# Kernel tuning notes

Hardware: AMD Instinct MI355X
Metric: run time of the kernel (lower is better)

## Reference

```python
import jax, jax.numpy as jnp
import numpy as np

N, E, DIN, DH, H, L = 8192, 32768, 1024, 256, 8, 3
NEG_SLOPE = 0.2  # PyG GATv2Conv default


def setup_inputs() -> dict:
    key = jax.random.key(0)
    ks = jax.random.split(key, 16)
    s = 0.05
    p = {}
    p["x"] = jax.random.normal(ks[0], (N, DIN), jnp.float32)
    p["edge_index"] = jax.random.randint(ks[1], (2, E), 0, N, jnp.int32)
    p["edge_attr"] = jax.random.randint(ks[2], (E,), 0, 5, jnp.int32)
    p["node_types"] = jax.random.randint(ks[3], (N,), 0, 5, jnp.int32)
    # input_proj (input_dim != hidden_dim so it is a Linear)
    p["W_in"] = jax.random.normal(ks[4], (DIN, DH), jnp.float32) * s
    p["b_in"] = jnp.zeros((DH,), jnp.float32)
    p["node_emb"] = jax.random.normal(ks[5], (5, DH), jnp.float32) * s
    p["edge_emb"] = jax.random.normal(ks[6], (5, DH), jnp.float32) * s
    # per-layer GATv2 params, stacked over L layers
    p["Wl"] = jax.random.normal(ks[7], (L, DH, H * DH), jnp.float32) * s   # lin_l
    p["bl"] = jnp.zeros((L, H * DH), jnp.float32)
    p["Wr"] = jax.random.normal(ks[8], (L, DH, H * DH), jnp.float32) * s   # lin_r
    p["br"] = jnp.zeros((L, H * DH), jnp.float32)
    p["We"] = jax.random.normal(ks[9], (L, DH, H * DH), jnp.float32) * s   # lin_edge (no bias)
    p["att"] = jax.random.normal(ks[10], (L, H, DH), jnp.float32) * s
    p["b_gat"] = jnp.zeros((L, DH), jnp.float32)                            # out bias (concat=False)
    p["W_out"] = jax.random.normal(ks[11], (DH, DH), jnp.float32) * s
    p["b_out"] = jnp.zeros((DH,), jnp.float32)
    return p


def _gatv2(h, src, dst, ea, Wl, bl, Wr, br, We, att, bias):
    n = h.shape[0]
    # add self loops; edge_attr fill_value='mean' = segment-mean of incoming edge attrs
    loop = jnp.arange(n, dtype=src.dtype)
    cnt = jax.ops.segment_sum(jnp.ones(dst.shape, jnp.float32), dst, num_segments=n)
    loop_ea = jax.ops.segment_sum(ea, dst, num_segments=n) / jnp.maximum(cnt, 1.0)[:, None]
    src2 = jnp.concatenate([src, loop])
    dst2 = jnp.concatenate([dst, loop])
    ea2 = jnp.concatenate([ea, loop_ea], axis=0)
    xl = (h @ Wl + bl).reshape(n, H, DH)   # source transform
    xr = (h @ Wr + br).reshape(n, H, DH)   # target transform
    ee = (ea2 @ We).reshape(-1, H, DH)     # edge transform [E2,H,C]
    z = jax.nn.leaky_relu(xl[src2] + xr[dst2] + ee, NEG_SLOPE)   # [E2,H,C]
    logits = jnp.einsum('ehc,hc->eh', z, att)                    # [E2,H]
    # numerically stable segment softmax over edges sharing a target node
    lmax = jax.ops.segment_max(logits, dst2, num_segments=n)     # [N,H]
    pnum = jnp.exp(logits - lmax[dst2])
    alpha = pnum / jax.ops.segment_sum(pnum, dst2, num_segments=n)[dst2]
    out = jax.ops.segment_sum(alpha[:, :, None] * xl[src2], dst2, num_segments=n)  # [N,H,C]
    return out.mean(axis=1) + bias          # concat=False -> head mean + bias


def reference(x, edge_index, edge_attr, node_types, W_in, b_in, node_emb, edge_emb,
              Wl, bl, Wr, br, We, att, b_gat, W_out, b_out):
    src, dst = edge_index[0], edge_index[1]
    h = x @ W_in + b_in + node_emb[node_types]
    for l in range(L):
        ea = edge_emb[edge_attr]
        h = jax.nn.relu(_gatv2(h, src, dst, ea, Wl[l], bl[l], Wr[l], br[l], We[l], att[l], b_gat[l]))
        # dropout p=0.1 is a no-op in eval mode
    return h @ W_out + b_out
```

## Files before the change

### kernel.cpp

```cpp
#include <hip/hip_runtime.h>

#define N_NODES 8192
#define N_EDGES 32768
#define D_IN    1024
#define DH      256
#define NH      8
#define HD      2048
#define NL      3
#define NT      5
#define NEG     0.2f

typedef __bf16 bf16x8 __attribute__((ext_vector_type(8)));
typedef float  f32x4  __attribute__((ext_vector_type(4)));
typedef unsigned short ushort8 __attribute__((ext_vector_type(8)));

static __device__ __forceinline__ unsigned short f2bf(float f) {
    unsigned u = __float_as_uint(f);
    unsigned r = (u + 0x7FFFu + ((u >> 16) & 1u)) >> 16;
    return (unsigned short)r;
}
static __device__ __forceinline__ float bf2f(unsigned short h) {
    return __uint_as_float(((unsigned)h) << 16);
}
static __device__ __forceinline__ void gload_lds16(const void* g, void* l) {
    __builtin_amdgcn_global_load_lds(
        (const __attribute__((address_space(1))) unsigned*)g,
        (__attribute__((address_space(3))) unsigned*)l, 16, 0, 0);
}

__global__ __launch_bounds__(256) void split_act8(
    const float* __restrict__ X, unsigned short* __restrict__ A3,
    int MK8, int k8shift)
{
    int idx = blockIdx.x * 256 + threadIdx.x;
    if (idx >= MK8) return;
    int K8 = 1 << k8shift;
    int K = K8 << 3;
    int m = idx >> k8shift, k8 = idx & (K8 - 1);
    const float* xp = X + (size_t)m * K + k8 * 8;
    float4 v0 = *(const float4*)xp;
    float4 v1 = *(const float4*)(xp + 4);
    float vv[8] = {v0.x, v0.y, v0.z, v0.w, v1.x, v1.y, v1.z, v1.w};
    ushort8 hi, lo;
#pragma unroll
    for (int j = 0; j < 8; j++) {
        unsigned short h = f2bf(vv[j]);
        hi[j] = h;
        lo[j] = f2bf(vv[j] - bf2f(h));
    }
    size_t b = (size_t)m * 3 * K + k8 * 8;
    *(ushort8*)(A3 + b)         = hi;
    *(ushort8*)(A3 + b + K)     = hi;
    *(ushort8*)(A3 + b + 2 * K) = lo;
}

__global__ __launch_bounds__(256) void split_w(
    const float* __restrict__ W, unsigned short* __restrict__ B3T,
    int K, int N)
{
    __shared__ float t[32][33];
    int k0 = blockIdx.y * 32, n0 = blockIdx.x * 32;
    int tid = threadIdx.x;
    int r = tid >> 5, c = tid & 31;
    for (int rr = r; rr < 32; rr += 8)
        t[rr][c] = W[(size_t)(k0 + rr) * N + n0 + c];
    __syncthreads();
    for (int rr = r; rr < 32; rr += 8) {
        int n = n0 + rr, k = k0 + c;
        float v = t[c][rr];
        unsigned short hu = f2bf(v);
        unsigned short lu = f2bf(v - bf2f(hu));
        size_t b = (size_t)n * 3 * K + k;
        B3T[b]         = hu;
        B3T[b + K]     = lu;
        B3T[b + 2 * K] = hu;
    }
}

__global__ __launch_bounds__(256) void init_c(
    float* __restrict__ C, const float* __restrict__ bias, int MN, int nshift,
    const float* __restrict__ emb, const int* __restrict__ types)
{
    for (int idx = blockIdx.x * 256 + threadIdx.x; idx < MN; idx += gridDim.x * 256) {
        int col = idx & ((1 << nshift) - 1);
        float v = bias[col];
        if (emb) v += emb[types[idx >> nshift] * DH + col];
        C[idx] = v;
    }
}

__global__ __launch_bounds__(256) void gemm_mfma(
    const unsigned short* __restrict__ A3, const unsigned short* __restrict__ B3T,
    const float* __restrict__ bias, float* __restrict__ C,
    int M, int N, int K3, int kslice)
{
    __shared__ unsigned short aLds[128 * 64];
    __shared__ unsigned short bLds[128 * 64];
    const int tid = threadIdx.x;
    const int m0 = blockIdx.y * 128, n0 = blockIdx.x * 128;
    const int lane = tid & 63, w = tid >> 6;
    const int wm = w >> 1, wn = w & 1;
    const int srow8 = lane >> 3;
    const int schunk = lane & 7;
    const int frow = lane & 15, fchunk = lane >> 4;
    const int kt0 = blockIdx.z * kslice;
    const int kt1 = kt0 + kslice;

    f32x4 acc[4][4] = {};

    for (int kt = kt0; kt < kt1; kt += 64) {
#pragma unroll
        for (int q = 0; q < 4; q++) {
            int row = (q * 4 + w) * 8 + srow8;
            int scol = (schunk << 4) ^ ((row & 7) << 4);
            char* ldst_a = (char*)aLds + (q * 4 + w) * 1024;
            char* ldst_b = (char*)bLds + (q * 4 + w) * 1024;
            gload_lds16(A3 + (size_t)(m0 + row) * K3 + kt + (scol >> 1), ldst_a);
            gload_lds16(B3T + (size_t)(n0 + row) * K3 + kt + (scol >> 1), ldst_b);
        }
        __syncthreads();
#pragma unroll
        for (int kh = 0; kh < 2; kh++) {
            const int c = kh * 4 + fchunk;
            bf16x8 af[4], bfr[4];
#pragma unroll
            for (int f = 0; f < 4; f++) {
                int ra = wm * 64 + f * 16 + frow;
                af[f] = *(const bf16x8*)((const char*)aLds + ra * 128 + ((c ^ (ra & 7)) << 4));
                int rb = wn * 64 + f * 16 + frow;
                bfr[f] = *(const bf16x8*)((const char*)bLds + rb * 128 + ((c ^ (rb & 7)) << 4));
            }
#pragma unroll
            for (int i = 0; i < 4; i++)
#pragma unroll
                for (int j = 0; j < 4; j++)
                    acc[i][j] = __builtin_amdgcn_mfma_f32_16x16x32_bf16(
                        af[i], bfr[j], acc[i][j], 0, 0, 0);
        }
        __syncthreads();
    }

    const int ccol = lane & 15, crq = (lane >> 4) * 4;
    if (gridDim.z == 1) {
#pragma unroll
        for (int j = 0; j < 4; j++) {
            int gcol = n0 + wn * 64 + j * 16 + ccol;
            float bv = bias[gcol];
#pragma unroll
            for (int i = 0; i < 4; i++)
#pragma unroll
                for (int r = 0; r < 4; r++) {
                    int grow = m0 + wm * 64 + i * 16 + crq + r;
                    C[(size_t)grow * N + gcol] = acc[i][j][r] + bv;
                }
        }
    } else {
#pragma unroll
        for (int j = 0; j < 4; j++) {
            int gcol = n0 + wn * 64 + j * 16 + ccol;
#pragma unroll
            for (int i = 0; i < 4; i++)
#pragma unroll
                for (int r = 0; r < 4; r++) {
                    int grow = m0 + wm * 64 + i * 16 + crq + r;
                    atomicAdd(&C[(size_t)grow * N + gcol], acc[i][j][r]);
                }
        }
    }
}

__global__ __launch_bounds__(256) void e5_kernel(
    const float* __restrict__ eemb, const float* __restrict__ We,
    float* __restrict__ E5)
{
    int col = blockIdx.x * 256 + threadIdx.x;
    int t = blockIdx.y;
    float acc = 0.f;
    for (int k = 0; k < DH; k++) acc += eemb[t * DH + k] * We[(size_t)k * HD + col];
    E5[(size_t)t * HD + col] = acc;
}

__global__ void deg_hist(const int* __restrict__ dst, const int* __restrict__ attr,
                         int* cnt, int* hist)
{
    int e = blockIdx.x * 256 + threadIdx.x;
    if (e < N_EDGES) {
        int d = dst[e];
        atomicAdd(&cnt[d], 1);
        atomicAdd(&hist[d * NT + attr[e]], 1);
    }
}

__global__ __launch_bounds__(256) void scan_kernel(const int* __restrict__ cnt,
                                                   int* __restrict__ rowptr)
{
    __shared__ int part[256];
    int tid = threadIdx.x;
    int base = tid * 32, s = 0;
    for (int i = 0; i < 32; i++) s += cnt[base + i];
    part[tid] = s;
    __syncthreads();
    for (int off = 1; off < 256; off <<= 1) {
        int v = (tid >= off) ? part[tid - off] : 0;
        __syncthreads();
        part[tid] += v;
        __syncthreads();
    }
    int run = (tid == 0) ? 0 : part[tid - 1];
    for (int i = 0; i < 32; i++) { rowptr[base + i] = run; run += cnt[base + i]; }
    if (tid == 255) rowptr[N_NODES] = run;
}

__global__ void csr_fill(const int* __restrict__ dst, const int* __restrict__ rowptr,
                         int* fillc, int* __restrict__ csr)
{
    int e = blockIdx.x * 256 + threadIdx.x;
    if (e < N_EDGES) {
        int d = dst[e];
        int p = atomicAdd(&fillc[d], 1);
        csr[rowptr[d] + p] = e;
    }
}

__global__ __launch_bounds__(256) void gat_online(
    const float* __restrict__ xl, const float* __restrict__ xr,
    const float* __restrict__ E5, const float* __restrict__ att,
    const int* __restrict__ csr, const int* __restrict__ rowptr,
    const int* __restrict__ cnt, const int* __restrict__ src,
    const int* __restrict__ attr, const int* __restrict__ hist,
    const float* __restrict__ bgat, float* __restrict__ hout)
{
    const int n = blockIdx.x, tid = threadIdx.x;
    const int h = tid >> 5, cb = tid & 31;
    const int base = h * DH + cb * 8;
    __shared__ float outs[NH][DH];

    const int deg = cnt[n];
    const int r0 = rowptr[n];

    float4 xr0 = *(const float4*)(xr + (size_t)n * HD + base);
    float4 xr1 = *(const float4*)(xr + (size_t)n * HD + base + 4);
    float4 at0 = *(const float4*)(att + base);
    float4 at1 = *(const float4*)(att + base + 4);

    float m = -1e30f, d = 0.f;
    float O0 = 0.f, O1 = 0.f, O2 = 0.f, O3 = 0.f;
    float O4 = 0.f, O5 = 0.f, O6 = 0.f, O7 = 0.f;

    for (int i = 0; i <= deg; i++) {
        const bool isloop = (i == deg);
        int s, a = 0;
        if (isloop) { s = n; }
        else { int e = csr[r0 + i]; s = src[e]; a = attr[e]; }

        const float* xp = xl + (size_t)s * HD + base;
        float4 v0 = *(const float4*)xp;
        float4 v1 = *(const float4*)(xp + 4);

        float4 e0, e1;
        if (isloop) {
            float inv = 1.f / fmaxf((float)deg, 1.f);
            e0 = make_float4(0.f, 0.f, 0.f, 0.f);
            e1 = make_float4(0.f, 0.f, 0.f, 0.f);
#pragma unroll
            for (int t = 0; t < NT; t++) {
                float wt = inv * (float)hist[n * NT + t];
                float4 q0 = *(const float4*)(E5 + (size_t)t * HD + base);
                float4 q1 = *(const float4*)(E5 + (size_t)t * HD + base + 4);
                e0.x += wt * q0.x; e0.y += wt * q0.y; e0.z += wt * q0.z; e0.w += wt * q0.w;
                e1.x += wt * q1.x; e1.y += wt * q1.y; e1.z += wt * q1.z; e1.w += wt * q1.w;
            }
        } else {
            e0 = *(const float4*)(E5 + (size_t)a * HD + base);
            e1 = *(const float4*)(E5 + (size_t)a * HD + base + 4);
        }

        float z, lsum = 0.f;
        z = v0.x + xr0.x + e0.x; z = (z >= 0.f) ? z : NEG * z; lsum += z * at0.x;
        z = v0.y + xr0.y + e0.y; z = (z >= 0.f) ? z : NEG * z; lsum += z * at0.y;
        z = v0.z + xr0.z + e0.z; z = (z >= 0.f) ? z : NEG * z; lsum += z * at0.z;
        z = v0.w + xr0.w + e0.w; z = (z >= 0.f) ? z : NEG * z; lsum += z * at0.w;
        z = v1.x + xr1.x + e1.x; z = (z >= 0.f) ? z : NEG * z; lsum += z * at1.x;
        z = v1.y + xr1.y + e1.y; z = (z >= 0.f) ? z : NEG * z; lsum += z * at1.y;
        z = v1.z + xr1.z + e1.z; z = (z >= 0.f) ? z : NEG * z; lsum += z * at1.z;
        z = v1.w + xr1.w + e1.w; z = (z >= 0.f) ? z : NEG * z; lsum += z * at1.w;

#pragma unroll
        for (int off = 16; off; off >>= 1) lsum += __shfl_xor(lsum, off, 32);

        float nm = fmaxf(m, lsum);
        float scale = __expf(m - nm);
        float p = __expf(lsum - nm);
        O0 = O0 * scale + p * v0.x; O1 = O1 * scale + p * v0.y;
        O2 = O2 * scale + p * v0.z; O3 = O3 * scale + p * v0.w;
        O4 = O4 * scale + p * v1.x; O5 = O5 * scale + p * v1.y;
        O6 = O6 * scale + p * v1.z; O7 = O7 * scale + p * v1.w;
        d = d * scale + p;
        m = nm;
    }

    float invd = 1.f / d;
    float4 w0 = make_float4(O0 * invd, O1 * invd, O2 * invd, O3 * invd);
    float4 w1 = make_float4(O4 * invd, O5 * invd, O6 * invd, O7 * invd);
    *(float4*)(&outs[h][cb * 8])     = w0;
    *(float4*)(&outs[h][cb * 8 + 4]) = w1;
    __syncthreads();

    float o = 0.f;
#pragma unroll
    for (int hh = 0; hh < NH; hh++) o += outs[hh][tid];
    o = o * 0.125f + bgat[tid];
    hout[(size_t)n * DH + tid] = fmaxf(o, 0.f);
}

extern "C" void kernel_launch(void* const* d_in, const int* in_sizes, int n_in,
                              void* d_out, int out_size, void* d_ws, size_t ws_size,
                              hipStream_t stream)
{
    const float* x     = (const float*)d_in[0];
    const int*   eidx  = (const int*)d_in[1];
    const int*   src   = eidx;
    const int*   dst   = eidx + N_EDGES;
    const int*   attr  = (const int*)d_in[2];
    const int*   types = (const int*)d_in[3];
    const float* W_in  = (const float*)d_in[4];
    const float* b_in  = (const float*)d_in[5];
    const float* nemb  = (const float*)d_in[6];
    const float* eemb  = (const float*)d_in[7];
    const float* Wl    = (const float*)d_in[8];
    const float* bl    = (const float*)d_in[9];
    const float* Wr    = (const float*)d_in[10];
    const float* br    = (const float*)d_in[11];
    const float* We    = (const float*)d_in[12];
    const float* att   = (const float*)d_in[13];
    const float* bgat  = (const float*)d_in[14];
    const float* W_out = (const float*)d_in[15];
    const float* b_out = (const float*)d_in[16];
    float* out = (float*)d_out;

    char* ws = (char*)d_ws;
    size_t off = 0;
    auto alloc = [&](size_t bytes) -> void* {
        void* p = ws + off;
        off += (bytes + 255) & ~(size_t)255;
        return p;
    };
    float* h      = (float*)alloc((size_t)N_NODES * DH * 4);
    float* xl     = (float*)alloc((size_t)N_NODES * HD * 4);
    float* xr     = (float*)alloc((size_t)N_NODES * HD * 4);
    float* E5     = (float*)alloc((size_t)NT * HD * 4);
    int* cnt      = (int*)alloc((size_t)N_NODES * 4);
    int* hist     = (int*)alloc((size_t)N_NODES * NT * 4);
    int* rowptr   = (int*)alloc((size_t)(N_NODES + 1) * 4);
    int* fillc    = (int*)alloc((size_t)N_NODES * 4);
    int* csr      = (int*)alloc((size_t)N_EDGES * 4);
    unsigned short* A3  = (unsigned short*)alloc((size_t)N_NODES * 3 * D_IN * 2);
    unsigned short* B3T = (unsigned short*)alloc((size_t)HD * 3 * D_IN * 2);

    hipMemsetAsync(cnt, 0, (size_t)N_NODES * 4, stream);
    hipMemsetAsync(hist, 0, (size_t)N_NODES * NT * 4, stream);
    hipMemsetAsync(fillc, 0, (size_t)N_NODES * 4, stream);

    deg_hist<<<(N_EDGES + 255) / 256, 256, 0, stream>>>(dst, attr, cnt, hist);
    scan_kernel<<<1, 256, 0, stream>>>(cnt, rowptr);
    csr_fill<<<(N_EDGES + 255) / 256, 256, 0, stream>>>(dst, rowptr, fillc, csr);

    split_act8<<<(N_NODES * D_IN / 8 + 255) / 256, 256, 0, stream>>>(
        x, A3, N_NODES * D_IN / 8, 7);
    split_w<<<dim3(DH / 32, D_IN / 32), 256, 0, stream>>>(W_in, B3T, D_IN, DH);
    init_c<<<2048, 256, 0, stream>>>(h, b_in, N_NODES * DH, 8, nemb, types);
    gemm_mfma<<<dim3(DH / 128, N_NODES / 128, 8), 256, 0, stream>>>(
        A3, B3T, nullptr, h, N_NODES, DH, 3 * D_IN, 3 * D_IN / 8);

    for (int l = 0; l < NL; l++) {
        const float* Wl_l = Wl + (size_t)l * DH * HD;
        const float* Wr_l = Wr + (size_t)l * DH * HD;
        const float* We_l = We + (size_t)l * DH * HD;

        split_act8<<<(N_NODES * DH / 8 + 255) / 256, 256, 0, stream>>>(
            h, A3, N_NODES * DH / 8, 5);
        split_w<<<dim3(HD / 32, DH / 32), 256, 0, stream>>>(Wl_l, B3T, DH, HD);
        gemm_mfma<<<dim3(HD / 128, N_NODES / 128, 1), 256, 0, stream>>>(
            A3, B3T, bl + (size_t)l * HD, xl, N_NODES, HD, 3 * DH, 3 * DH);
        split_w<<<dim3(HD / 32, DH / 32), 256, 0, stream>>>(Wr_l, B3T, DH, HD);
        gemm_mfma<<<dim3(HD / 128, N_NODES / 128, 1), 256, 0, stream>>>(
            A3, B3T, br + (size_t)l * HD, xr, N_NODES, HD, 3 * DH, 3 * DH);

        e5_kernel<<<dim3(HD / 256, NT), 256, 0, stream>>>(eemb, We_l, E5);
        gat_online<<<N_NODES, 256, 0, stream>>>(
            xl, xr, E5, att + (size_t)l * NH * DH, csr, rowptr, cnt, src, attr,
            hist, bgat + (size_t)l * DH, h);
    }

    split_act8<<<(N_NODES * DH / 8 + 255) / 256, 256, 0, stream>>>(
        h, A3, N_NODES * DH / 8, 5);
    split_w<<<dim3(DH / 32, DH / 32), 256, 0, stream>>>(W_out, B3T, DH, DH);
    init_c<<<2048, 256, 0, stream>>>(out, b_out, N_NODES * DH, 8, nullptr, nullptr);
    gemm_mfma<<<dim3(DH / 128, N_NODES / 128, 4), 256, 0, stream>>>(
        A3, B3T, nullptr, out, N_NODES, DH, 3 * DH, 3 * DH / 4);
}
```

Baseline: 805.0 us.

## Fuse lin_l and lin_r GEMMs and prefetch next neighbor in GAT aggregation

Concatenates the Wl and Wr projections into a single GEMM producing an interleaved [N, 4096] xl|xr buffer, with per-column bias selection, removing one GEMM launch per layer. The GAT online-softmax loop now loads the next neighbor's xl features before computing the current edge, overlapping gather latency with arithmetic. This costs extra registers and a wider row stride in the gathered buffer.

```diff
diff --git a/kernel.cpp b/kernel.cpp
--- a/kernel.cpp
+++ b/kernel.cpp
@@ -6,6 +6,7 @@
 #define DH      256
 #define NH      8
 #define HD      2048
+#define W2      4096
 #define NL      3
 #define NT      5
 #define NEG     0.2f
@@ -91,8 +92,8 @@
 
 __global__ __launch_bounds__(256) void gemm_mfma(
     const unsigned short* __restrict__ A3, const unsigned short* __restrict__ B3T,
-    const float* __restrict__ bias, float* __restrict__ C,
-    int M, int N, int K3, int kslice)
+    const float* __restrict__ bias, const float* __restrict__ bias2, int nsplit,
+    float* __restrict__ C, int M, int N, int K3, int kslice)
 {
     __shared__ unsigned short aLds[128 * 64];
     __shared__ unsigned short bLds[128 * 64];
@@ -145,7 +146,7 @@
 #pragma unroll
         for (int j = 0; j < 4; j++) {
             int gcol = n0 + wn * 64 + j * 16 + ccol;
-            float bv = bias[gcol];
+            float bv = (gcol < nsplit) ? bias[gcol] : bias2[gcol - nsplit];
 #pragma unroll
             for (int i = 0; i < 4; i++)
 #pragma unroll
@@ -223,12 +224,12 @@
 }
 
 __global__ __launch_bounds__(256) void gat_online(
-    const float* __restrict__ xl, const float* __restrict__ xr,
-    const float* __restrict__ E5, const float* __restrict__ att,
-    const int* __restrict__ csr, const int* __restrict__ rowptr,
-    const int* __restrict__ cnt, const int* __restrict__ src,
-    const int* __restrict__ attr, const int* __restrict__ hist,
-    const float* __restrict__ bgat, float* __restrict__ hout)
+    const float* __restrict__ xlr, const float* __restrict__ E5,
+    const float* __restrict__ att, const int* __restrict__ csr,
+    const int* __restrict__ rowptr, const int* __restrict__ cnt,
+    const int* __restrict__ src, const int* __restrict__ attr,
+    const int* __restrict__ hist, const float* __restrict__ bgat,
+    float* __restrict__ hout)
 {
     const int n = blockIdx.x, tid = threadIdx.x;
     const int h = tid >> 5, cb = tid & 31;
@@ -238,8 +239,8 @@
     const int deg = cnt[n];
     const int r0 = rowptr[n];
 
-    float4 xr0 = *(const float4*)(xr + (size_t)n * HD + base);
-    float4 xr1 = *(const float4*)(xr + (size_t)n * HD + base + 4);
+    float4 xr0 = *(const float4*)(xlr + (size_t)n * W2 + HD + base);
+    float4 xr1 = *(const float4*)(xlr + (size_t)n * W2 + HD + base + 4);
     float4 at0 = *(const float4*)(att + base);
     float4 at1 = *(const float4*)(att + base + 4);
 
@@ -247,43 +248,53 @@
     float O0 = 0.f, O1 = 0.f, O2 = 0.f, O3 = 0.f;
     float O4 = 0.f, O5 = 0.f, O6 = 0.f, O7 = 0.f;
 
+    int a_c;
+    int s_c;
+    if (deg == 0) { s_c = n; a_c = -1; }
+    else { int e0 = csr[r0]; s_c = src[e0]; a_c = attr[e0]; }
+    const float* xp = xlr + (size_t)s_c * W2 + base;
+    float4 v0 = *(const float4*)xp;
+    float4 v1 = *(const float4*)(xp + 4);
+
     for (int i = 0; i <= deg; i++) {
-        const bool isloop = (i == deg);
-        int s, a = 0;
-        if (isloop) { s = n; }
-        else { int e = csr[r0 + i]; s = src[e]; a = attr[e]; }
-
-        const float* xp = xl + (size_t)s * HD + base;
-        float4 v0 = *(const float4*)xp;
-        float4 v1 = *(const float4*)(xp + 4);
-
-        float4 e0, e1;
-        if (isloop) {
+        int a_n = 0;
+        float4 n0 = make_float4(0.f, 0.f, 0.f, 0.f), n1 = n0;
+        if (i < deg) {
+            int s_n;
+            if (i + 1 == deg) { s_n = n; a_n = -1; }
+            else { int e = csr[r0 + i + 1]; s_n = src[e]; a_n = attr[e]; }
+            const float* xq = xlr + (size_t)s_n * W2 + base;
+            n0 = *(const float4*)xq;
+            n1 = *(const float4*)(xq + 4);
+        }
+
+        float4 e0v, e1v;
+        if (a_c < 0) {
             float inv = 1.f / fmaxf((float)deg, 1.f);
-            e0 = make_float4(0.f, 0.f, 0.f, 0.f);
-            e1 = make_float4(0.f, 0.f, 0.f, 0.f);
+            e0v = make_float4(0.f, 0.f, 0.f, 0.f);
+            e1v = make_float4(0.f, 0.f, 0.f, 0.f);
 #pragma unroll
             for (int t = 0; t < NT; t++) {
                 float wt = inv * (float)hist[n * NT + t];
                 float4 q0 = *(const float4*)(E5 + (size_t)t * HD + base);
                 float4 q1 = *(const float4*)(E5 + (size_t)t * HD + base + 4);
-                e0.x += wt * q0.x; e0.y += wt * q0.y; e0.z += wt * q0.z; e0.w += wt * q0.w;
-                e1.x += wt * q1.x; e1.y += wt * q1.y; e1.z += wt * q1.z; e1.w += wt * q1.w;
+                e0v.x += wt * q0.x; e0v.y += wt * q0.y; e0v.z += wt * q0.z; e0v.w += wt * q0.w;
+                e1v.x += wt * q1.x; e1v.y += wt * q1.y; e1v.z += wt * q1.z; e1v.w += wt * q1.w;
             }
         } else {
-            e0 = *(const float4*)(E5 + (size_t)a * HD + base);
-            e1 = *(const float4*)(E5 + (size_t)a * HD + base + 4);
+            e0v = *(const float4*)(E5 + (size_t)a_c * HD + base);
+            e1v = *(const float4*)(E5 + (size_t)a_c * HD + base + 4);
         }
 
         float z, lsum = 0.f;
-        z = v0.x + xr0.x + e0.x; z = (z >= 0.f) ? z : NEG * z; lsum += z * at0.x;
-        z = v0.y + xr0.y + e0.y; z = (z >= 0.f) ? z : NEG * z; lsum += z * at0.y;
-        z = v0.z + xr0.z + e0.z; z = (z >= 0.f) ? z : NEG * z; lsum += z * at0.z;
-        z = v0.w + xr0.w + e0.w; z = (z >= 0.f) ? z : NEG * z; lsum += z * at0.w;
-        z = v1.x + xr1.x + e1.x; z = (z >= 0.f) ? z : NEG * z; lsum += z * at1.x;
-        z = v1.y + xr1.y + e1.y; z = (z >= 0.f) ? z : NEG * z; lsum += z * at1.y;
-        z = v1.z + xr1.z + e1.z; z = (z >= 0.f) ? z : NEG * z; lsum += z * at1.z;
-        z = v1.w + xr1.w + e1.w; z = (z >= 0.f) ? z : NEG * z; lsum += z * at1.w;
+        z = v0.x + xr0.x + e0v.x; z = (z >= 0.f) ? z : NEG * z; lsum += z * at0.x;
+        z = v0.y + xr0.y + e0v.y; z = (z >= 0.f) ? z : NEG * z; lsum += z * at0.y;
+        z = v0.z + xr0.z + e0v.z; z = (z >= 0.f) ? z : NEG * z; lsum += z * at0.z;
+        z = v0.w + xr0.w + e0v.w; z = (z >= 0.f) ? z : NEG * z; lsum += z * at0.w;
+        z = v1.x + xr1.x + e1v.x; z = (z >= 0.f) ? z : NEG * z; lsum += z * at1.x;
+        z = v1.y + xr1.y + e1v.y; z = (z >= 0.f) ? z : NEG * z; lsum += z * at1.y;
+        z = v1.z + xr1.z + e1v.z; z = (z >= 0.f) ? z : NEG * z; lsum += z * at1.z;
+        z = v1.w + xr1.w + e1v.w; z = (z >= 0.f) ? z : NEG * z; lsum += z * at1.w;
 
 #pragma unroll
         for (int off = 16; off; off >>= 1) lsum += __shfl_xor(lsum, off, 32);
@@ -297,6 +308,8 @@
         O6 = O6 * scale + p * v1.z; O7 = O7 * scale + p * v1.w;
         d = d * scale + p;
         m = nm;
+
+        v0 = n0; v1 = n1; a_c = a_n;
     }
 
     float invd = 1.f / d;
@@ -346,8 +359,7 @@
         return p;
     };
     float* h      = (float*)alloc((size_t)N_NODES * DH * 4);
-    float* xl     = (float*)alloc((size_t)N_NODES * HD * 4);
-    float* xr     = (float*)alloc((size_t)N_NODES * HD * 4);
+    float* xlr    = (float*)alloc((size_t)N_NODES * W2 * 4);
     float* E5     = (float*)alloc((size_t)NT * HD * 4);
     int* cnt      = (int*)alloc((size_t)N_NODES * 4);
     int* hist     = (int*)alloc((size_t)N_NODES * NT * 4);
@@ -355,7 +367,8 @@
     int* fillc    = (int*)alloc((size_t)N_NODES * 4);
     int* csr      = (int*)alloc((size_t)N_EDGES * 4);
     unsigned short* A3  = (unsigned short*)alloc((size_t)N_NODES * 3 * D_IN * 2);
-    unsigned short* B3T = (unsigned short*)alloc((size_t)HD * 3 * D_IN * 2);
+    unsigned short* B3T = (unsigned short*)alloc((size_t)W2 * 3 * DH * 2 +
+                                                 (size_t)DH * 3 * D_IN * 2);
 
     hipMemsetAsync(cnt, 0, (size_t)N_NODES * 4, stream);
     hipMemsetAsync(hist, 0, (size_t)N_NODES * NT * 4, stream);
@@ -370,7 +383,7 @@
     split_w<<<dim3(DH / 32, D_IN / 32), 256, 0, stream>>>(W_in, B3T, D_IN, DH);
     init_c<<<2048, 256, 0, stream>>>(h, b_in, N_NODES * DH, 8, nemb, types);
     gemm_mfma<<<dim3(DH / 128, N_NODES / 128, 8), 256, 0, stream>>>(
-        A3, B3T, nullptr, h, N_NODES, DH, 3 * D_IN, 3 * D_IN / 8);
+        A3, B3T, nullptr, nullptr, DH, h, N_NODES, DH, 3 * D_IN, 3 * D_IN / 8);
 
     for (int l = 0; l < NL; l++) {
         const float* Wl_l = Wl + (size_t)l * DH * HD;
@@ -380,15 +393,15 @@
         split_act8<<<(N_NODES * DH / 8 + 255) / 256, 256, 0, stream>>>(
             h, A3, N_NODES * DH / 8, 5);
         split_w<<<dim3(HD / 32, DH / 32), 256, 0, stream>>>(Wl_l, B3T, DH, HD);
-        gemm_mfma<<<dim3(HD / 128, N_NODES / 128, 1), 256, 0, stream>>>(
-            A3, B3T, bl + (size_t)l * HD, xl, N_NODES, HD, 3 * DH, 3 * DH);
-        split_w<<<dim3(HD / 32, DH / 32), 256, 0, stream>>>(Wr_l, B3T, DH, HD);
-        gemm_mfma<<<dim3(HD / 128, N_NODES / 128, 1), 256, 0, stream>>>(
-            A3, B3T, br + (size_t)l * HD, xr, N_NODES, HD, 3 * DH, 3 * DH);
+        split_w<<<dim3(HD / 32, DH / 32), 256, 0, stream>>>(
+            Wr_l, B3T + (size_t)HD * 3 * DH, DH, HD);
+        gemm_mfma<<<dim3(W2 / 128, N_NODES / 128, 1), 256, 0, stream>>>(
+            A3, B3T, bl + (size_t)l * HD, br + (size_t)l * HD, HD,
+            xlr, N_NODES, W2, 3 * DH, 3 * DH);
 
         e5_kernel<<<dim3(HD / 256, NT), 256, 0, stream>>>(eemb, We_l, E5);
         gat_online<<<N_NODES, 256, 0, stream>>>(
-            xl, xr, E5, att + (size_t)l * NH * DH, csr, rowptr, cnt, src, attr,
+            xlr, E5, att + (size_t)l * NH * DH, csr, rowptr, cnt, src, attr,
             hist, bgat + (size_t)l * DH, h);
     }
 
@@ -397,5 +410,5 @@
     split_w<<<dim3(DH / 32, DH / 32), 256, 0, stream>>>(W_out, B3T, DH, DH);
     init_c<<<2048, 256, 0, stream>>>(out, b_out, N_NODES * DH, 8, nullptr, nullptr);
     gemm_mfma<<<dim3(DH / 128, N_NODES / 128, 4), 256, 0, stream>>>(
-        A3, B3T, nullptr, out, N_NODES, DH, 3 * DH, 3 * DH / 4);
-}
+        A3, B3T, nullptr, nullptr, DH, out, N_NODES, DH, 3 * DH, 3 * DH / 4);
+}
```

Result: faster. 785.6 us (-2.4%).
